# Performance work log

Measured on AMD Instinct MI355X. Metric: run time of the kernel, lower is better.

The kernel has to match this reference:

```python
import jax, jax.numpy as jnp
import numpy as np

M, K, N = 8192, 4096, 4096

def setup_inputs() -> dict:
    key = jax.random.key(0)
    k1, k2, k3, k4, k5 = jax.random.split(key, 5)
    # int8-range quantized tensors stored as int32 (int8 values in [-128, 127])
    inp = jax.random.randint(k1, (M, K), -128, 128, dtype=jnp.int32)
    weight = jax.random.randint(k2, (N, K), -128, 128, dtype=jnp.int32)
    bias = jax.random.normal(k3, (N,), dtype=jnp.float32)
    inp_scales = jax.random.uniform(k4, (1,), jnp.float32, 0.01, 0.05)        # per-tensor
    inp_zero_points = jnp.zeros((1,), jnp.int32)                               # symmetric
    weight_scales = jax.random.uniform(k5, (N,), jnp.float32, 0.005, 0.02)     # per-channel
    weight_zero_points = jnp.zeros((N,), jnp.int32)
    return {
        "inp": inp, "weight": weight, "bias": bias,
        "inp_scales": inp_scales, "inp_zero_points": inp_zero_points,
        "weight_scales": weight_scales, "weight_zero_points": weight_zero_points,
    }

def reference(inp, weight, bias, inp_scales, inp_zero_points, weight_scales, weight_zero_points):
    # qdq_linear fallback path: dequantize activation (per-tensor) and weight
    # (per-output-channel), fp32 matmul, add bias. output_dtype=float32,
    # output_scales/zero_points=None => no output requantization.
    x = (inp.astype(jnp.float32) - inp_zero_points.astype(jnp.float32)) * inp_scales  # [M,K]
    w = (weight.astype(jnp.float32) - weight_zero_points[:, None].astype(jnp.float32)) \
        * weight_scales[:, None]                                                      # [N,K]
    return jnp.einsum('mk,nk->mn', x, w) + bias                                       # [M,N]
```

## Files before the change

### kernel.cpp

```cpp
#include <hip/hip_runtime.h>

#define MM 8192
#define NN 4096
#define KK 4096

#define BM 128
#define BN 128
#define BK 128

typedef int int32x4 __attribute__((ext_vector_type(4)));

__device__ __forceinline__ void async_load16(const void* g, void* l) {
  __builtin_amdgcn_global_load_lds(
      (__attribute__((address_space(1))) void*)(void*)g,
      (__attribute__((address_space(3))) void*)l,
      16, 0, 0);
}

__global__ __launch_bounds__(256) void pack_kernel(
    const int* __restrict__ a, const int* __restrict__ w,
    char* __restrict__ a8, char* __restrict__ w8,
    const int* __restrict__ izp, const int* __restrict__ wzp) {
  const long tid = (long)blockIdx.x * 256 + threadIdx.x;
  const long A_T = (long)MM * KK / 4;

  const int4* src;
  int* dst;
  int z;
  if (tid < A_T) {
    src = (const int4*)a + tid;
    dst = (int*)a8 + tid;
    z = izp[0];
  } else {
    long t = tid - A_T;
    src = (const int4*)w + t;
    dst = (int*)w8 + t;
    z = wzp[t >> 10];
  }

  int4 v = *src;
  union { char c[4]; int q; } u;
  u.c[0] = (char)(v.x - z);
  u.c[1] = (char)(v.y - z);
  u.c[2] = (char)(v.z - z);
  u.c[3] = (char)(v.w - z);
  *dst = u.q;
}

__global__ __launch_bounds__(256, 2) void qgemm_kernel(
    const char* __restrict__ A8, const char* __restrict__ W8,
    float* __restrict__ out,
    const float* __restrict__ bias,
    const float* __restrict__ is_ptr,
    const float* __restrict__ wscale) {
  __shared__ __attribute__((aligned(16))) char As[BM * BK];
  __shared__ __attribute__((aligned(16))) char Bs[BN * BK];

  int pid = blockIdx.x;
  pid = (pid & 7) * 256 + (pid >> 3);
  const int group  = pid >> 8;
  const int within = pid & 255;
  const int bm = group * 8 + (within & 7);
  const int bn = within >> 3;

  const int tid  = threadIdx.x;
  const int wave = tid >> 6;
  const int lane = tid & 63;
  const int wm = (wave >> 1) * 64;
  const int wn = (wave & 1) * 64;

  const int srow = lane >> 3;
  const int ssub = (lane & 7) ^ srow;
  const char* a_src[4];
  const char* b_src[4];
  char* a_dst[4];
  char* b_dst[4];
#pragma unroll
  for (int j = 0; j < 4; ++j) {
    const int c = wave + j * 4;
    a_src[j] = A8 + (long)(bm * BM + c * 8 + srow) * KK + ssub * 16;
    b_src[j] = W8 + (long)(bn * BN + c * 8 + srow) * KK + ssub * 16;
    a_dst[j] = As + c * 1024;
    b_dst[j] = Bs + c * 1024;
  }

  const int row_q = lane & 15;
  const int quad  = lane >> 4;
  const int psub0 = quad ^ (row_q & 7);
  const int psub1 = psub0 ^ 4;
  const char* a_rd = As + (wm + row_q) * BK;
  const char* b_rd = Bs + (wn + row_q) * BK;

  int32x4 acc[4][4];
#pragma unroll
  for (int mi = 0; mi < 4; ++mi)
#pragma unroll
    for (int ni = 0; ni < 4; ++ni) acc[mi][ni] = (int32x4)0;

  for (int kk = 0; kk < KK; kk += BK) {
#pragma unroll
    for (int j = 0; j < 4; ++j) {
      async_load16(a_src[j] + kk, a_dst[j]);
      async_load16(b_src[j] + kk, b_dst[j]);
    }
    __syncthreads();

#pragma unroll
    for (int h = 0; h < 2; ++h) {
      const int ps = (h == 0) ? psub0 : psub1;
      int32x4 afrag[4], bfrag[4];
#pragma unroll
      for (int mi = 0; mi < 4; ++mi)
        afrag[mi] = *(const int32x4*)(a_rd + mi * 16 * BK + ps * 16);
#pragma unroll
      for (int ni = 0; ni < 4; ++ni)
        bfrag[ni] = *(const int32x4*)(b_rd + ni * 16 * BK + ps * 16);

#pragma unroll
      for (int mi = 0; mi < 4; ++mi)
#pragma unroll
        for (int ni = 0; ni < 4; ++ni)
          acc[mi][ni] = __builtin_amdgcn_mfma_i32_16x16x64_i8(
              afrag[mi], bfrag[ni], acc[mi][ni], 0, 0, 0);
    }

    __syncthreads();
  }

  const float is0 = is_ptr[0];
  const int row_base = bm * BM + wm + quad * 4;
  const int col_base = bn * BN + wn + row_q;
#pragma unroll
  for (int ni = 0; ni < 4; ++ni) {
    const int col = col_base + ni * 16;
    const float s = is0 * wscale[col];
    const float b = bias[col];
#pragma unroll
    for (int mi = 0; mi < 4; ++mi) {
      const int row = row_base + mi * 16;
#pragma unroll
      for (int r = 0; r < 4; ++r) {
        out[(long)(row + r) * NN + col] = (float)acc[mi][ni][r] * s + b;
      }
    }
  }
}

extern "C" void kernel_launch(void* const* d_in, const int* in_sizes, int n_in,
                              void* d_out, int out_size, void* d_ws, size_t ws_size,
                              hipStream_t stream) {
  const int*   inp    = (const int*)d_in[0];
  const int*   weight = (const int*)d_in[1];
  const float* bias   = (const float*)d_in[2];
  const float* iscale = (const float*)d_in[3];
  const int*   izp    = (const int*)d_in[4];
  const float* wscale = (const float*)d_in[5];
  const int*   wzp    = (const int*)d_in[6];
  float* out = (float*)d_out;

  char* a8 = (char*)d_ws;
  char* w8 = a8 + (size_t)MM * KK;

  pack_kernel<<<49152, 256, 0, stream>>>(inp, weight, a8, w8, izp, wzp);

  qgemm_kernel<<<2048, 256, 0, stream>>>(a8, w8, out, bias, iscale, wscale);
}
```

Before: 403.8 us.

## Pre-swizzle int8 operands into MFMA fragment layout and load directly to registers

The pack kernel now writes A and W int8 data in a tiled layout that matches the 32x32x32 i8 MFMA operand fragments. This lets the GEMM kernel drop shared memory and barriers entirely and load fragments straight from global memory into registers with a software-pipelined register double-buffer. Occupancy is raised to 3 blocks per CU. The trade-off is no LDS reuse across waves: each wave fetches its own A and B fragments from global memory or L2, which raises cache traffic.

Measured after the change: 447.3 us. 10.8% more time.

```diff
diff --git a/kernel.cpp b/kernel.cpp
--- a/kernel.cpp
+++ b/kernel.cpp
@@ -6,37 +6,38 @@
 
 #define BM 128
 #define BN 128
-#define BK 128
 
-typedef int int32x4 __attribute__((ext_vector_type(4)));
-
-__device__ __forceinline__ void async_load16(const void* g, void* l) {
-  __builtin_amdgcn_global_load_lds(
-      (__attribute__((address_space(1))) void*)(void*)g,
-      (__attribute__((address_space(3))) void*)l,
-      16, 0, 0);
-}
+typedef int int32x4  __attribute__((ext_vector_type(4)));
+typedef int int32x16 __attribute__((ext_vector_type(16)));
 
 __global__ __launch_bounds__(256) void pack_kernel(
     const int* __restrict__ a, const int* __restrict__ w,
-    char* __restrict__ a8, char* __restrict__ w8,
+    char* __restrict__ a8s, char* __restrict__ b8s,
     const int* __restrict__ izp, const int* __restrict__ wzp) {
   const long tid = (long)blockIdx.x * 256 + threadIdx.x;
   const long A_T = (long)MM * KK / 4;
 
   const int4* src;
-  int* dst;
-  int z;
+  int* dstbase;
+  long row;
+  int r4, z;
   if (tid < A_T) {
     src = (const int4*)a + tid;
-    dst = (int*)a8 + tid;
+    dstbase = (int*)a8s;
+    row = tid >> 10;
+    r4  = (int)(tid & 1023);
     z = izp[0];
   } else {
-    long t = tid - A_T;
+    const long t = tid - A_T;
     src = (const int4*)w + t;
-    dst = (int*)w8 + t;
-    z = wzp[t >> 10];
+    dstbase = (int*)b8s;
+    row = t >> 10;
+    r4  = (int)(t & 1023);
+    z = wzp[row];
   }
+  const int  ks = r4 >> 3;
+  const int  l  = ((int)row & 31) + (((r4 >> 2) & 1) << 5);
+  const long didx = ((((row >> 5) << 7) + ks) << 8) + l * 4 + (r4 & 3);
 
   int4 v = *src;
   union { char c[4]; int q; } u;
@@ -44,24 +45,19 @@
   u.c[1] = (char)(v.y - z);
   u.c[2] = (char)(v.z - z);
   u.c[3] = (char)(v.w - z);
-  *dst = u.q;
+  dstbase[didx] = u.q;
 }
 
-__global__ __launch_bounds__(256, 2) void qgemm_kernel(
-    const char* __restrict__ A8, const char* __restrict__ W8,
+__global__ __launch_bounds__(256, 3) void qgemm_kernel(
+    const char* __restrict__ A8S, const char* __restrict__ B8S,
     float* __restrict__ out,
     const float* __restrict__ bias,
     const float* __restrict__ is_ptr,
     const float* __restrict__ wscale) {
-  __shared__ __attribute__((aligned(16))) char As[BM * BK];
-  __shared__ __attribute__((aligned(16))) char Bs[BN * BK];
-
   int pid = blockIdx.x;
   pid = (pid & 7) * 256 + (pid >> 3);
-  const int group  = pid >> 8;
-  const int within = pid & 255;
-  const int bm = group * 8 + (within & 7);
-  const int bn = within >> 3;
+  const int bm = (pid >> 8) * 8 + (pid & 7);
+  const int bn = (pid & 255) >> 3;
 
   const int tid  = threadIdx.x;
   const int wave = tid >> 6;
@@ -69,78 +65,77 @@
   const int wm = (wave >> 1) * 64;
   const int wn = (wave & 1) * 64;
 
-  const int srow = lane >> 3;
-  const int ssub = (lane & 7) ^ srow;
-  const char* a_src[4];
-  const char* b_src[4];
-  char* a_dst[4];
-  char* b_dst[4];
-#pragma unroll
-  for (int j = 0; j < 4; ++j) {
-    const int c = wave + j * 4;
-    a_src[j] = A8 + (long)(bm * BM + c * 8 + srow) * KK + ssub * 16;
-    b_src[j] = W8 + (long)(bn * BN + c * 8 + srow) * KK + ssub * 16;
-    a_dst[j] = As + c * 1024;
-    b_dst[j] = Bs + c * 1024;
-  }
+  const int mt0 = bm * 4 + (wm >> 5);
+  const int nt0 = bn * 4 + (wn >> 5);
+  const int lo  = lane * 16;
+  const char* aB0 = A8S + ((long)(mt0    ) << 17) + lo;
+  const char* aB1 = A8S + ((long)(mt0 + 1) << 17) + lo;
+  const char* bB0 = B8S + ((long)(nt0    ) << 17) + lo;
+  const char* bB1 = B8S + ((long)(nt0 + 1) << 17) + lo;
 
-  const int row_q = lane & 15;
-  const int quad  = lane >> 4;
-  const int psub0 = quad ^ (row_q & 7);
-  const int psub1 = psub0 ^ 4;
-  const char* a_rd = As + (wm + row_q) * BK;
-  const char* b_rd = Bs + (wn + row_q) * BK;
+#define LD(base, k) (*(const int32x4*)((base) + ((long)(k) << 5)))
+#define MFMA(a, b, c) __builtin_amdgcn_mfma_i32_32x32x32_i8((a), (b), (c), 0, 0, 0)
 
-  int32x4 acc[4][4];
-#pragma unroll
-  for (int mi = 0; mi < 4; ++mi)
-#pragma unroll
-    for (int ni = 0; ni < 4; ++ni) acc[mi][ni] = (int32x4)0;
+  int32x16 acc00 = (int32x16)0, acc01 = (int32x16)0;
+  int32x16 acc10 = (int32x16)0, acc11 = (int32x16)0;
 
-  for (int kk = 0; kk < KK; kk += BK) {
-#pragma unroll
-    for (int j = 0; j < 4; ++j) {
-      async_load16(a_src[j] + kk, a_dst[j]);
-      async_load16(b_src[j] + kk, b_dst[j]);
-    }
-    __syncthreads();
+  int32x4 a0[2], b0[2], a1[2], b1[2], a2[2], b2[2], a3[2], b3[2];
+  a0[0] = LD(aB0, 0);  a0[1] = LD(aB1, 0);
+  b0[0] = LD(bB0, 0);  b0[1] = LD(bB1, 0);
+  a1[0] = LD(aB0, 32); a1[1] = LD(aB1, 32);
+  b1[0] = LD(bB0, 32); b1[1] = LD(bB1, 32);
 
-#pragma unroll
-    for (int h = 0; h < 2; ++h) {
-      const int ps = (h == 0) ? psub0 : psub1;
-      int32x4 afrag[4], bfrag[4];
-#pragma unroll
-      for (int mi = 0; mi < 4; ++mi)
-        afrag[mi] = *(const int32x4*)(a_rd + mi * 16 * BK + ps * 16);
-#pragma unroll
-      for (int ni = 0; ni < 4; ++ni)
-        bfrag[ni] = *(const int32x4*)(b_rd + ni * 16 * BK + ps * 16);
+  for (int kk = 0; kk < KK; kk += 128) {
+    const int k2 = kk + 64;
+    a2[0] = LD(aB0, k2); a2[1] = LD(aB1, k2);
+    b2[0] = LD(bB0, k2); b2[1] = LD(bB1, k2);
+    acc00 = MFMA(a0[0], b0[0], acc00);
+    acc01 = MFMA(a0[0], b0[1], acc01);
+    acc10 = MFMA(a0[1], b0[0], acc10);
+    acc11 = MFMA(a0[1], b0[1], acc11);
 
-#pragma unroll
-      for (int mi = 0; mi < 4; ++mi)
-#pragma unroll
-        for (int ni = 0; ni < 4; ++ni)
-          acc[mi][ni] = __builtin_amdgcn_mfma_i32_16x16x64_i8(
-              afrag[mi], bfrag[ni], acc[mi][ni], 0, 0, 0);
-    }
+    const int k3 = kk + 96;
+    a3[0] = LD(aB0, k3); a3[1] = LD(aB1, k3);
+    b3[0] = LD(bB0, k3); b3[1] = LD(bB1, k3);
+    acc00 = MFMA(a1[0], b1[0], acc00);
+    acc01 = MFMA(a1[0], b1[1], acc01);
+    acc10 = MFMA(a1[1], b1[0], acc10);
+    acc11 = MFMA(a1[1], b1[1], acc11);
 
-    __syncthreads();
+    const int k4 = (kk + 128 < KK) ? kk + 128 : 0;
+    a0[0] = LD(aB0, k4); a0[1] = LD(aB1, k4);
+    b0[0] = LD(bB0, k4); b0[1] = LD(bB1, k4);
+    acc00 = MFMA(a2[0], b2[0], acc00);
+    acc01 = MFMA(a2[0], b2[1], acc01);
+    acc10 = MFMA(a2[1], b2[0], acc10);
+    acc11 = MFMA(a2[1], b2[1], acc11);
+
+    const int k5 = (kk + 160 < KK) ? kk + 160 : 0;
+    a1[0] = LD(aB0, k5); a1[1] = LD(aB1, k5);
+    b1[0] = LD(bB0, k5); b1[1] = LD(bB1, k5);
+    acc00 = MFMA(a3[0], b3[0], acc00);
+    acc01 = MFMA(a3[0], b3[1], acc01);
+    acc10 = MFMA(a3[1], b3[0], acc10);
+    acc11 = MFMA(a3[1], b3[1], acc11);
   }
 
   const float is0 = is_ptr[0];
-  const int row_base = bm * BM + wm + quad * 4;
-  const int col_base = bn * BN + wn + row_q;
+  const int colb = bn * BN + wn + (lane & 31);
+  const int rowb = bm * BM + wm + 4 * (lane >> 5);
 #pragma unroll
-  for (int ni = 0; ni < 4; ++ni) {
-    const int col = col_base + ni * 16;
+  for (int ni = 0; ni < 2; ++ni) {
+    const int col = colb + ni * 32;
     const float s = is0 * wscale[col];
-    const float b = bias[col];
+    const float bv = bias[col];
 #pragma unroll
-    for (int mi = 0; mi < 4; ++mi) {
-      const int row = row_base + mi * 16;
+    for (int mi = 0; mi < 2; ++mi) {
+      const int32x16 A = (mi == 0) ? (ni == 0 ? acc00 : acc01)
+                                   : (ni == 0 ? acc10 : acc11);
+      const int row0 = rowb + mi * 32;
 #pragma unroll
-      for (int r = 0; r < 4; ++r) {
-        out[(long)(row + r) * NN + col] = (float)acc[mi][ni][r] * s + b;
+      for (int r = 0; r < 16; ++r) {
+        const int row = row0 + (r & 3) + 8 * (r >> 2);
+        out[(long)row * NN + col] = (float)A[r] * s + bv;
       }
     }
   }
@@ -158,10 +153,10 @@
   const int*   wzp    = (const int*)d_in[6];
   float* out = (float*)d_out;
 
-  char* a8 = (char*)d_ws;
-  char* w8 = a8 + (size_t)MM * KK;
+  char* a8s = (char*)d_ws;
+  char* b8s = a8s + (size_t)MM * KK;
 
-  pack_kernel<<<49152, 256, 0, stream>>>(inp, weight, a8, w8, izp, wzp);
+  pack_kernel<<<49152, 256, 0, stream>>>(inp, weight, a8s, b8s, izp, wzp);
 
-  qgemm_kernel<<<2048, 256, 0, stream>>>(a8, w8, out, bias, iscale, wscale);
+  qgemm_kernel<<<2048, 256, 0, stream>>>(a8s, b8s, out, bias, iscale, wscale);
 }
```
